# Optimization experiments

Hardware: AMD Instinct MI355X
Metric: run time of the kernel (lower is better)

The kernel has to match this reference:

```python
import jax, jax.numpy as jnp
import numpy as np

N_ENEMY = 4_000_000
N_GUN = 1_000_000
N_EDGES = 16_000_000
HID = 64
OUT = 8


def setup_inputs() -> dict:
    key = jax.random.key(0)
    ks = jax.random.split(key, 9)
    x_enemy = jax.random.normal(ks[0], (N_ENEMY, 4), dtype=jnp.float32)
    x_gun = jax.random.normal(ks[1], (N_GUN, 1), dtype=jnp.float32)
    edge_src = jax.random.randint(ks[2], (N_EDGES,), 0, N_ENEMY, dtype=jnp.int64 if jax.config.jax_enable_x64 else jnp.int32)
    edge_dst = jax.random.randint(ks[3], (N_EDGES,), 0, N_GUN, dtype=jnp.int64 if jax.config.jax_enable_x64 else jnp.int32)
    W_l = jax.random.normal(ks[4], (4, HID), dtype=jnp.float32) * 0.5
    b_l = jax.random.normal(ks[5], (HID,), dtype=jnp.float32) * 0.1
    W_r = jax.random.normal(ks[6], (1, HID), dtype=jnp.float32) * 0.5
    W_fc = jax.random.normal(ks[7], (HID, OUT), dtype=jnp.float32) * 0.1
    b_fc = jax.random.normal(ks[8], (OUT,), dtype=jnp.float32) * 0.1
    return {"x_enemy": x_enemy, "x_gun": x_gun, "edge_src": edge_src,
            "edge_dst": edge_dst, "W_l": W_l, "b_l": b_l, "W_r": W_r,
            "W_fc": W_fc, "b_fc": b_fc}


def reference(x_enemy, x_gun, edge_src, edge_dst, W_l, b_l, W_r, W_fc, b_fc):
    n_gun = x_gun.shape[0]
    # gather enemy messages along edges: [E, 4]
    msgs = x_enemy[edge_src]
    # mean aggregation per gun node (zero for isolated nodes, like PyG scatter-mean)
    summed = jax.ops.segment_sum(msgs, edge_dst, num_segments=n_gun)  # [N_gun, 4]
    counts = jax.ops.segment_sum(jnp.ones((edge_dst.shape[0],), dtype=x_enemy.dtype),
                                 edge_dst, num_segments=n_gun)       # [N_gun]
    mean = summed / jnp.maximum(counts, 1.0)[:, None]
    # SAGEConv: lin_l(aggr) + lin_r(x_dst)  (lin_l has bias, lin_r bias-free)
    h = mean @ W_l + b_l + x_gun @ W_r                                # [N_gun, HID]
    # linear head -> q values
    return h @ W_fc + b_fc                                            # [N_gun, OUT]
```

## Files before the change

kernel.cpp:

```cpp
#include <hip/hip_runtime.h>

#define N_ENEMY 4000000
#define N_GUN   1000000
#define N_EDGES 16000000
#define OUTD    8

#define NB   1024
#define GPB  977
#define T8   8192
#define NT8  1954
#define EPT8 32

#define CH   4096
#define CEPT 16

__device__ __forceinline__ unsigned int bucket_of(unsigned int dst) {
    return (unsigned int)(((unsigned long long)dst * 1125395730ull) >> 40);
}
__device__ __forceinline__ unsigned int rne_bf16(unsigned int u) {
    return (u + 0x7FFFu + ((u >> 16) & 1u)) >> 16;
}

__global__ void prep_params(const float* __restrict__ W_l, const float* __restrict__ b_l,
                            const float* __restrict__ W_r, const float* __restrict__ W_fc,
                            const float* __restrict__ b_fc, float* __restrict__ P) {
    int o = threadIdx.x;
    if (o < OUTD) {
        float a0 = 0.f, a1 = 0.f, a2 = 0.f, a3 = 0.f, r = 0.f, c = 0.f;
        for (int h = 0; h < 64; ++h) {
            float w = W_fc[h * OUTD + o];
            a0 += W_l[0 * 64 + h] * w;
            a1 += W_l[1 * 64 + h] * w;
            a2 += W_l[2 * 64 + h] * w;
            a3 += W_l[3 * 64 + h] * w;
            r  += W_r[h] * w;
            c  += b_l[h] * w;
        }
        P[0 * OUTD + o] = a0;
        P[1 * OUTD + o] = a1;
        P[2 * OUTD + o] = a2;
        P[3 * OUTD + o] = a3;
        P[4 * OUTD + o] = r;
        P[5 * OUTD + o] = c + b_fc[o];
    }
}

__global__ void conv_kernel(const uint4* __restrict__ xe, uint2* __restrict__ xeb) {
    int i = blockIdx.x * blockDim.x + threadIdx.x;
    if (i >= N_ENEMY) return;
    uint4 v = xe[i];
    uint2 q;
    q.x = rne_bf16(v.x) | (rne_bf16(v.y) << 16);
    q.y = rne_bf16(v.z) | (rne_bf16(v.w) << 16);
    xeb[i] = q;
}

__global__ void hist2_kernel(const int* __restrict__ edst, unsigned short* __restrict__ tileh) {
    __shared__ unsigned int lh[NB];
    int t = threadIdx.x;
    for (int i = t; i < NB; i += 256) lh[i] = 0;
    __syncthreads();
    int ebase = blockIdx.x * T8;
    int nE = N_EDGES - ebase;
    if (nE > T8) nE = T8;
    for (int i = t; i < nE; i += 256)
        atomicAdd(&lh[bucket_of((unsigned)edst[ebase + i])], 1u);
    __syncthreads();
    unsigned short* row = tileh + (size_t)blockIdx.x * NB;
    for (int i = t; i < NB; i += 256) row[i] = (unsigned short)lh[i];
}

template<int K>
__global__ __launch_bounds__(256)
void tile_scanT(unsigned short* __restrict__ tileh, unsigned int* __restrict__ tot,
                int nbk, int ntile) {
    __shared__ unsigned int part[256][17];
    int t = threadIdx.x;
    int b0 = blockIdx.x * 16;
    unsigned int loc[16];
#pragma unroll
    for (int j = 0; j < 16; ++j) loc[j] = 0;
    for (int k = 0; k < K; ++k) {
        int tile = t * K + k;
        if (tile < ntile) {
            const unsigned short* row = tileh + (size_t)tile * nbk + b0;
#pragma unroll
            for (int j = 0; j < 16; ++j) loc[j] += row[j];
        }
    }
#pragma unroll
    for (int j = 0; j < 16; ++j) part[t][j] = loc[j];
    __syncthreads();
    if (t < 16) {
        unsigned int acc = 0;
        for (int i = 0; i < 256; ++i) {
            unsigned int v = part[i][t];
            part[i][t] = acc;
            acc += v;
        }
        tot[b0 + t] = acc;
    }
    __syncthreads();
    unsigned int run[16];
#pragma unroll
    for (int j = 0; j < 16; ++j) run[j] = part[t][j];
    for (int k = 0; k < K; ++k) {
        int tile = t * K + k;
        if (tile < ntile) {
            unsigned short* row = tileh + (size_t)tile * nbk + b0;
#pragma unroll
            for (int j = 0; j < 16; ++j) {
                unsigned int c = row[j];
                row[j] = (unsigned short)run[j];
                run[j] += c;
            }
        }
    }
}

__global__ void scan_kernel(const unsigned int* __restrict__ tot,
                            unsigned int* __restrict__ offsets) {
    __shared__ unsigned int tmp[1024];
    int t = threadIdx.x;
    unsigned int v0 = (t < NB) ? tot[t] : 0u;
    tmp[t] = v0;
    __syncthreads();
    for (int d = 1; d < 1024; d <<= 1) {
        unsigned int v = (t >= d) ? tmp[t - d] : 0u;
        __syncthreads();
        tmp[t] += v;
        __syncthreads();
    }
    if (t < NB) offsets[t] = tmp[t] - v0;
    if (t == NB - 1) offsets[NB] = tmp[t];
}

__global__ __launch_bounds__(256, 2)
void scatter_sorted(const int* __restrict__ esrc, const int* __restrict__ edst,
                    const unsigned int* __restrict__ offsets,
                    const unsigned short* __restrict__ tileh,
                    unsigned int* __restrict__ payload) {
    __shared__ unsigned int cnt[NB];
    __shared__ unsigned int base[NB];
    __shared__ unsigned int gb[NB];
    __shared__ unsigned short bOf[T8];
    __shared__ unsigned int sorted[T8];
    __shared__ unsigned int partial[256];
    int t = threadIdx.x;
    int tile = blockIdx.x;
    int ebase = tile * T8;
    int nE = N_EDGES - ebase;
    if (nE > T8) nE = T8;
    for (int i = t; i < NB; i += 256) cnt[i] = 0;
    __syncthreads();
    unsigned int w[EPT8];
    unsigned int br[EPT8];
#pragma unroll
    for (int k = 0; k < EPT8; ++k) {
        int idx = k * 256 + t;
        if (idx < nE) {
            unsigned int s = (unsigned int)esrc[ebase + idx];
            unsigned int d = (unsigned int)edst[ebase + idx];
            unsigned int b = bucket_of(d);
            unsigned int g = d - b * GPB;
            unsigned int r = atomicAdd(&cnt[b], 1u);
            w[k]  = (s << 10) | g;
            br[k] = (b << 13) | r;
        } else br[k] = 0xFFFFFFFFu;
    }
    __syncthreads();
    unsigned int loc[4];
    unsigned int s = 0;
#pragma unroll
    for (int j = 0; j < 4; ++j) {
        int b = t * 4 + j;
        unsigned int c = cnt[b];
        loc[j] = s; s += c;
    }
    partial[t] = s;
    __syncthreads();
    for (int d = 1; d < 256; d <<= 1) {
        unsigned int v = (t >= d) ? partial[t - d] : 0u;
        __syncthreads();
        partial[t] += v;
        __syncthreads();
    }
    unsigned int excl = (t > 0) ? partial[t - 1] : 0u;
#pragma unroll
    for (int j = 0; j < 4; ++j) base[t * 4 + j] = excl + loc[j];
    __syncthreads();
    const unsigned short* trow = tileh + (size_t)tile * NB;
#pragma unroll
    for (int j = 0; j < 4; ++j) {
        int b = t * 4 + j;
        gb[b] = offsets[b] + (unsigned int)trow[b];
        unsigned int bs = base[b];
        unsigned int c = cnt[b];
        for (unsigned int p = bs; p < bs + c; ++p) bOf[p] = (unsigned short)b;
    }
    __syncthreads();
#pragma unroll
    for (int k = 0; k < EPT8; ++k) {
        if (br[k] != 0xFFFFFFFFu) {
            unsigned int b = br[k] >> 13;
            unsigned int r = br[k] & 8191u;
            sorted[base[b] + r] = w[k];
        }
    }
    __syncthreads();
    for (int p = t; p < nE; p += 256) {
        unsigned int b = bOf[p];
        payload[gb[b] + ((unsigned int)p - base[b])] = sorted[p];
    }
}

__global__ __launch_bounds__(256)
void bucket_v9(const unsigned int* __restrict__ offsets,
               const unsigned int* __restrict__ payload,
               const uint2* __restrict__ xeb,
               const float* __restrict__ xg,
               const float* __restrict__ P,
               float* __restrict__ out) {
    __shared__ unsigned long long sorted[CH];
    __shared__ unsigned int cnt[1024];
    __shared__ unsigned int base_[1024];
    __shared__ unsigned int partial[256];
    __shared__ float sP[48];
    int t = threadIdx.x;
    if (t < 48) sP[t] = P[t];
    __syncthreads();

    float a0[4] = {0,0,0,0}, a1[4] = {0,0,0,0}, a2[4] = {0,0,0,0}, a3[4] = {0,0,0,0};
    float an[4] = {0,0,0,0};

    unsigned int b = blockIdx.x;
    unsigned int segS = offsets[b], segE = offsets[b + 1];

    for (unsigned int cs = segS; cs < segE; cs += CH) {
        int n = (int)((segE - cs < (unsigned int)CH) ? (segE - cs) : (unsigned int)CH);
        for (int i = t; i < 1024; i += 256) cnt[i] = 0;
        __syncthreads();

        unsigned int g_[CEPT], r_[CEPT];
        uint2 q_[CEPT];
#pragma unroll
        for (int k = 0; k < CEPT; ++k) {
            int idx = k * 256 + t;
            if (idx < n) {
                unsigned int p = payload[cs + idx];
                q_[k] = xeb[p >> 10];
                unsigned int g = p & 1023u;
                g_[k] = g;
                r_[k] = atomicAdd(&cnt[g], 1u);
            } else g_[k] = 0xFFFFFFFFu;
        }
        __syncthreads();

        unsigned int loc[4];
        unsigned int acc = 0;
#pragma unroll
        for (int j = 0; j < 4; ++j) {
            loc[j] = acc; acc += cnt[t * 4 + j];
        }
        partial[t] = acc;
        __syncthreads();
        for (int d = 1; d < 256; d <<= 1) {
            unsigned int v = (t >= d) ? partial[t - d] : 0u;
            __syncthreads();
            partial[t] += v;
            __syncthreads();
        }
        unsigned int excl = (t > 0) ? partial[t - 1] : 0u;
#pragma unroll
        for (int j = 0; j < 4; ++j) base_[t * 4 + j] = excl + loc[j];
        __syncthreads();

#pragma unroll
        for (int k = 0; k < CEPT; ++k) {
            if (g_[k] != 0xFFFFFFFFu) {
                sorted[base_[g_[k]] + r_[k]] =
                    ((unsigned long long)q_[k].y << 32) | (unsigned long long)q_[k].x;
            }
        }
        __syncthreads();

#pragma unroll
        for (int j = 0; j < 4; ++j) {
            int g = j * 256 + t;
            unsigned int bs = base_[g], c = cnt[g];
            for (unsigned int p2 = bs; p2 < bs + c; ++p2) {
                unsigned long long v = sorted[p2];
                unsigned int lo = (unsigned int)v, hi = (unsigned int)(v >> 32);
                a0[j] += __uint_as_float(lo << 16);
                a1[j] += __uint_as_float(lo & 0xffff0000u);
                a2[j] += __uint_as_float(hi << 16);
                a3[j] += __uint_as_float(hi & 0xffff0000u);
            }
            an[j] += (float)c;
        }
        __syncthreads();
    }

#pragma unroll
    for (int j = 0; j < 4; ++j) {
        int g = j * 256 + t;
        if (g >= GPB) continue;
        unsigned int G = b * GPB + (unsigned int)g;
        if (G >= N_GUN) continue;
        float inv = 1.0f / fmaxf(an[j], 1.0f);
        float m0 = a0[j] * inv, m1 = a1[j] * inv, m2 = a2[j] * inv, m3 = a3[j] * inv;
        float xv = xg[G];
        float res[OUTD];
#pragma unroll
        for (int o = 0; o < OUTD; ++o) {
            res[o] = m0 * sP[o] + m1 * sP[8 + o] + m2 * sP[16 + o] + m3 * sP[24 + o]
                   + xv * sP[32 + o] + sP[40 + o];
        }
        float4* op = (float4*)(out + (size_t)G * OUTD);
        op[0] = make_float4(res[0], res[1], res[2], res[3]);
        op[1] = make_float4(res[4], res[5], res[6], res[7]);
    }
}

__global__ void edge_kernel(const int4* __restrict__ esrc4, const int4* __restrict__ edst4,
                            const float4* __restrict__ xe, float* __restrict__ summed,
                            float* __restrict__ counts) {
    int t = blockIdx.x * blockDim.x + threadIdx.x;
    if (t >= N_EDGES / 4) return;
    int4 s4 = esrc4[t];
    int4 d4 = edst4[t];
    int ss[4] = { s4.x, s4.y, s4.z, s4.w };
    int dd[4] = { d4.x, d4.y, d4.z, d4.w };
#pragma unroll
    for (int k = 0; k < 4; ++k) {
        float4 m = xe[ss[k]];
        float* basep = summed + (size_t)dd[k] * 4;
        atomicAdd(basep + 0, m.x);
        atomicAdd(basep + 1, m.y);
        atomicAdd(basep + 2, m.z);
        atomicAdd(basep + 3, m.w);
        atomicAdd(counts + dd[k], 1.0f);
    }
}

__global__ void gun_kernel(const float4* __restrict__ summed, const float* __restrict__ counts,
                           const float* __restrict__ xg, const float* __restrict__ P,
                           float* __restrict__ out) {
    __shared__ float sP[48];
    if (threadIdx.x < 48) sP[threadIdx.x] = P[threadIdx.x];
    __syncthreads();
    int g = blockIdx.x * blockDim.x + threadIdx.x;
    if (g >= N_GUN) return;
    float4 s = summed[g];
    float cnt = counts[g];
    float inv = 1.0f / fmaxf(cnt, 1.0f);
    float m0 = s.x * inv, m1 = s.y * inv, m2 = s.z * inv, m3 = s.w * inv;
    float xv = xg[g];
    float res[OUTD];
#pragma unroll
    for (int o = 0; o < OUTD; ++o) {
        res[o] = m0 * sP[o] + m1 * sP[8 + o] + m2 * sP[16 + o] + m3 * sP[24 + o]
               + xv * sP[32 + o] + sP[40 + o];
    }
    float4* op = (float4*)(out + (size_t)g * OUTD);
    op[0] = make_float4(res[0], res[1], res[2], res[3]);
    op[1] = make_float4(res[4], res[5], res[6], res[7]);
}

extern "C" void kernel_launch(void* const* d_in, const int* in_sizes, int n_in,
                              void* d_out, int out_size, void* d_ws, size_t ws_size,
                              hipStream_t stream) {
    const float* x_enemy = (const float*)d_in[0];
    const float* x_gun   = (const float*)d_in[1];
    const int*   esrc    = (const int*)d_in[2];
    const int*   edst    = (const int*)d_in[3];
    const float* W_l     = (const float*)d_in[4];
    const float* b_l     = (const float*)d_in[5];
    const float* W_r     = (const float*)d_in[6];
    const float* W_fc    = (const float*)d_in[7];
    const float* b_fc    = (const float*)d_in[8];
    float* out = (float*)d_out;

    const size_t PAYLOAD_OFF = 0;
    const size_t XEB_OFF     = (size_t)N_EDGES;
    const size_t TOT_OFF     = XEB_OFF + (size_t)N_ENEMY*2;
    const size_t OFFS_OFF    = TOT_OFF + NB;
    const size_t P_OFF       = OFFS_OFF + NB + 1;
    const size_t NEEDED_FULL = (P_OFF + 64) * sizeof(unsigned int);

    if (ws_size >= NEEDED_FULL) {
        unsigned int*   ws      = (unsigned int*)d_ws;
        unsigned int*   payload = ws + PAYLOAD_OFF;
        uint2*          xeb     = (uint2*)(ws + XEB_OFF);
        unsigned short* tileh   = (unsigned short*)(ws + XEB_OFF);
        unsigned int*   tot     = ws + TOT_OFF;
        unsigned int*   offsets = ws + OFFS_OFF;
        float*          P       = (float*)(ws + P_OFF);

        prep_params<<<1, 64, 0, stream>>>(W_l, b_l, W_r, W_fc, b_fc, P);
        hist2_kernel<<<NT8, 256, 0, stream>>>(edst, tileh);
        tile_scanT<8><<<NB / 16, 256, 0, stream>>>(tileh, tot, NB, NT8);
        scan_kernel<<<1, 1024, 0, stream>>>(tot, offsets);
        scatter_sorted<<<NT8, 256, 0, stream>>>(esrc, edst, offsets, tileh, payload);
        conv_kernel<<<(N_ENEMY + 255) / 256, 256, 0, stream>>>((const uint4*)x_enemy, xeb);
        bucket_v9<<<NB, 256, 0, stream>>>(offsets, payload, xeb, x_gun, P, out);
    } else {
        float* summed = (float*)d_ws;
        float* counts = summed + (size_t)N_GUN * 4;
        float* P      = counts + N_GUN;
        hipMemsetAsync(d_ws, 0, ((size_t)N_GUN * 5 + 48) * sizeof(float), stream);
        prep_params<<<1, 64, 0, stream>>>(W_l, b_l, W_r, W_fc, b_fc, P);
        int edge_threads = N_EDGES / 4;
        edge_kernel<<<(edge_threads + 255) / 256, 256, 0, stream>>>(
            (const int4*)esrc, (const int4*)edst, (const float4*)x_enemy, summed, counts);
        gun_kernel<<<(N_GUN + 255) / 256, 256, 0, stream>>>(
            (const float4*)summed, counts, x_gun, P, out);
    }
}
```

Measured before the change: 460.3 us.

## Partition bucket edges by source slice and rotate slice order per XCC

Adds a slice_sort kernel that reorders each bucket's payload into 8 slices keyed by the top bits of the source index. The gather kernel then walks the slices in an order rotated by the hardware XCC id. The intent is that blocks on the same XCC gather from the same region of the enemy feature table at the same time, which should improve L2 hit rates for the random gathers. The cost is an extra kernel that reads and writes the whole 16M-entry payload. Segments longer than the shared-memory capacity fall back to a single unsorted range.

```diff
diff --git a/kernel.cpp b/kernel.cpp
--- a/kernel.cpp
+++ b/kernel.cpp
@@ -14,11 +14,19 @@
 #define CH   4096
 #define CEPT 16
 
+#define NS   8
+#define SEG_CAP 16128
+
 __device__ __forceinline__ unsigned int bucket_of(unsigned int dst) {
     return (unsigned int)(((unsigned long long)dst * 1125395730ull) >> 40);
 }
 __device__ __forceinline__ unsigned int rne_bf16(unsigned int u) {
     return (u + 0x7FFFu + ((u >> 16) & 1u)) >> 16;
+}
+__device__ __forceinline__ unsigned int get_xcc() {
+    unsigned int x;
+    asm("s_getreg_b32 %0, hwreg(HW_REG_XCC_ID)" : "=s"(x));
+    return x;
 }
 
 __global__ void prep_params(const float* __restrict__ W_l, const float* __restrict__ b_l,
@@ -215,7 +223,48 @@
 }
 
 __global__ __launch_bounds__(256)
-void bucket_v9(const unsigned int* __restrict__ offsets,
+void slice_sort(const unsigned int* __restrict__ offsets,
+                unsigned int* __restrict__ payload,
+                unsigned int* __restrict__ stab) {
+    __shared__ unsigned int A[SEG_CAP];
+    __shared__ unsigned int cnt[NS];
+    __shared__ unsigned int base[NS + 1];
+    int b = blockIdx.x;
+    int t = threadIdx.x;
+    unsigned int segS = offsets[b];
+    unsigned int segE = offsets[b + 1];
+    unsigned int len = segE - segS;
+    if (len > SEG_CAP) {
+        if (t <= NS) stab[b * (NS + 1) + t] = (t == 0) ? segS : segE;
+        return;
+    }
+    if (t < NS) cnt[t] = 0;
+    __syncthreads();
+    for (unsigned int i = t; i < len; i += 256) {
+        unsigned int w = payload[segS + i];
+        A[i] = w;
+        atomicAdd(&cnt[w >> 29], 1u);
+    }
+    __syncthreads();
+    if (t == 0) {
+        unsigned int acc = 0;
+        for (int k = 0; k < NS; ++k) { base[k] = acc; acc += cnt[k]; }
+        base[NS] = acc;
+    }
+    __syncthreads();
+    if (t < NS) cnt[t] = 0;
+    __syncthreads();
+    for (unsigned int i = t; i < len; i += 256) {
+        unsigned int w = A[i];
+        unsigned int k = w >> 29;
+        unsigned int r = atomicAdd(&cnt[k], 1u);
+        payload[segS + base[k] + r] = w;
+    }
+    if (t <= NS) stab[b * (NS + 1) + t] = segS + base[t];
+}
+
+__global__ __launch_bounds__(256)
+void bucket_v9(const unsigned int* __restrict__ stab,
                const unsigned int* __restrict__ payload,
                const uint2* __restrict__ xeb,
                const float* __restrict__ xg,
@@ -234,71 +283,77 @@
     float an[4] = {0,0,0,0};
 
     unsigned int b = blockIdx.x;
-    unsigned int segS = offsets[b], segE = offsets[b + 1];
-
-    for (unsigned int cs = segS; cs < segE; cs += CH) {
-        int n = (int)((segE - cs < (unsigned int)CH) ? (segE - cs) : (unsigned int)CH);
-        for (int i = t; i < 1024; i += 256) cnt[i] = 0;
-        __syncthreads();
-
-        unsigned int g_[CEPT], r_[CEPT];
-        uint2 q_[CEPT];
-#pragma unroll
-        for (int k = 0; k < CEPT; ++k) {
-            int idx = k * 256 + t;
-            if (idx < n) {
-                unsigned int p = payload[cs + idx];
-                q_[k] = xeb[p >> 10];
-                unsigned int g = p & 1023u;
-                g_[k] = g;
-                r_[k] = atomicAdd(&cnt[g], 1u);
-            } else g_[k] = 0xFFFFFFFFu;
-        }
-        __syncthreads();
-
-        unsigned int loc[4];
-        unsigned int acc = 0;
-#pragma unroll
-        for (int j = 0; j < 4; ++j) {
-            loc[j] = acc; acc += cnt[t * 4 + j];
-        }
-        partial[t] = acc;
-        __syncthreads();
-        for (int d = 1; d < 256; d <<= 1) {
-            unsigned int v = (t >= d) ? partial[t - d] : 0u;
-            __syncthreads();
-            partial[t] += v;
-            __syncthreads();
-        }
-        unsigned int excl = (t > 0) ? partial[t - 1] : 0u;
-#pragma unroll
-        for (int j = 0; j < 4; ++j) base_[t * 4 + j] = excl + loc[j];
-        __syncthreads();
-
-#pragma unroll
-        for (int k = 0; k < CEPT; ++k) {
-            if (g_[k] != 0xFFFFFFFFu) {
-                sorted[base_[g_[k]] + r_[k]] =
-                    ((unsigned long long)q_[k].y << 32) | (unsigned long long)q_[k].x;
-            }
-        }
-        __syncthreads();
-
-#pragma unroll
-        for (int j = 0; j < 4; ++j) {
-            int g = j * 256 + t;
-            unsigned int bs = base_[g], c = cnt[g];
-            for (unsigned int p2 = bs; p2 < bs + c; ++p2) {
-                unsigned long long v = sorted[p2];
-                unsigned int lo = (unsigned int)v, hi = (unsigned int)(v >> 32);
-                a0[j] += __uint_as_float(lo << 16);
-                a1[j] += __uint_as_float(lo & 0xffff0000u);
-                a2[j] += __uint_as_float(hi << 16);
-                a3[j] += __uint_as_float(hi & 0xffff0000u);
-            }
-            an[j] += (float)c;
-        }
-        __syncthreads();
+    unsigned int rot = get_xcc() & (NS - 1u);
+
+    for (int si = 0; si < NS; ++si) {
+        unsigned int s = ((unsigned int)si + rot) & (NS - 1u);
+        unsigned int rs = stab[b * (NS + 1) + s];
+        unsigned int re = stab[b * (NS + 1) + s + 1];
+
+        for (unsigned int cs = rs; cs < re; cs += CH) {
+            int n = (int)((re - cs < (unsigned int)CH) ? (re - cs) : (unsigned int)CH);
+            for (int i = t; i < 1024; i += 256) cnt[i] = 0;
+            __syncthreads();
+
+            unsigned int g_[CEPT], r_[CEPT];
+            uint2 q_[CEPT];
+#pragma unroll
+            for (int k = 0; k < CEPT; ++k) {
+                int idx = k * 256 + t;
+                if (idx < n) {
+                    unsigned int p = payload[cs + idx];
+                    q_[k] = xeb[p >> 10];
+                    unsigned int g = p & 1023u;
+                    g_[k] = g;
+                    r_[k] = atomicAdd(&cnt[g], 1u);
+                } else g_[k] = 0xFFFFFFFFu;
+            }
+            __syncthreads();
+
+            unsigned int loc[4];
+            unsigned int acc = 0;
+#pragma unroll
+            for (int j = 0; j < 4; ++j) {
+                loc[j] = acc; acc += cnt[t * 4 + j];
+            }
+            partial[t] = acc;
+            __syncthreads();
+            for (int d = 1; d < 256; d <<= 1) {
+                unsigned int v = (t >= d) ? partial[t - d] : 0u;
+                __syncthreads();
+                partial[t] += v;
+                __syncthreads();
+            }
+            unsigned int excl = (t > 0) ? partial[t - 1] : 0u;
+#pragma unroll
+            for (int j = 0; j < 4; ++j) base_[t * 4 + j] = excl + loc[j];
+            __syncthreads();
+
+#pragma unroll
+            for (int k = 0; k < CEPT; ++k) {
+                if (g_[k] != 0xFFFFFFFFu) {
+                    sorted[base_[g_[k]] + r_[k]] =
+                        ((unsigned long long)q_[k].y << 32) | (unsigned long long)q_[k].x;
+                }
+            }
+            __syncthreads();
+
+#pragma unroll
+            for (int j = 0; j < 4; ++j) {
+                int g = j * 256 + t;
+                unsigned int bs = base_[g], c = cnt[g];
+                for (unsigned int p2 = bs; p2 < bs + c; ++p2) {
+                    unsigned long long v = sorted[p2];
+                    unsigned int lo = (unsigned int)v, hi = (unsigned int)(v >> 32);
+                    a0[j] += __uint_as_float(lo << 16);
+                    a1[j] += __uint_as_float(lo & 0xffff0000u);
+                    a2[j] += __uint_as_float(hi << 16);
+                    a3[j] += __uint_as_float(hi & 0xffff0000u);
+                }
+                an[j] += (float)c;
+            }
+            __syncthreads();
+        }
     }
 
 #pragma unroll
@@ -386,7 +441,8 @@
     const size_t TOT_OFF     = XEB_OFF + (size_t)N_ENEMY*2;
     const size_t OFFS_OFF    = TOT_OFF + NB;
     const size_t P_OFF       = OFFS_OFF + NB + 1;
-    const size_t NEEDED_FULL = (P_OFF + 64) * sizeof(unsigned int);
+    const size_t STAB_OFF    = P_OFF + 48;
+    const size_t NEEDED_FULL = (STAB_OFF + (size_t)NB * (NS + 1) + 16) * sizeof(unsigned int);
 
     if (ws_size >= NEEDED_FULL) {
         unsigned int*   ws      = (unsigned int*)d_ws;
@@ -396,14 +452,16 @@
         unsigned int*   tot     = ws + TOT_OFF;
         unsigned int*   offsets = ws + OFFS_OFF;
         float*          P       = (float*)(ws + P_OFF);
+        unsigned int*   stab    = ws + STAB_OFF;
 
         prep_params<<<1, 64, 0, stream>>>(W_l, b_l, W_r, W_fc, b_fc, P);
         hist2_kernel<<<NT8, 256, 0, stream>>>(edst, tileh);
         tile_scanT<8><<<NB / 16, 256, 0, stream>>>(tileh, tot, NB, NT8);
         scan_kernel<<<1, 1024, 0, stream>>>(tot, offsets);
         scatter_sorted<<<NT8, 256, 0, stream>>>(esrc, edst, offsets, tileh, payload);
+        slice_sort<<<NB, 256, 0, stream>>>(offsets, payload, stab);
         conv_kernel<<<(N_ENEMY + 255) / 256, 256, 0, stream>>>((const uint4*)x_enemy, xeb);
-        bucket_v9<<<NB, 256, 0, stream>>>(offsets, payload, xeb, x_gun, P, out);
+        bucket_v9<<<NB, 256, 0, stream>>>(stab, payload, xeb, x_gun, P, out);
     } else {
         float* summed = (float*)d_ws;
         float* counts = summed + (size_t)N_GUN * 4;
```

Measured after the change: 413.5 us. 10.2% less time.
